# Kernel tuning notes

Hardware: AMD Instinct MI355X
Metric: run time of the kernel (lower is better)

Reference implementation:

```python
import jax, jax.numpy as jnp
import numpy as np

B, S, F, H, P = 2048, 168, 7, 128, 96  # batch, window, features, hidden, pred_len


def setup_inputs() -> dict:
    key = jax.random.key(0)
    ks = jax.random.split(key, 16)
    sc = 0.05
    return {
        "xb": jax.random.normal(ks[0], (B, S, F), dtype=jnp.float32),
        # encoder LSTM (1 layer, unidirectional); gate order i,f,g,o like torch
        "W_ih_enc": jax.random.normal(ks[1], (4 * H, F), dtype=jnp.float32) * sc,
        "W_hh_enc": jax.random.normal(ks[2], (4 * H, H), dtype=jnp.float32) * sc,
        "b_ih_enc": jax.random.normal(ks[3], (4 * H,), dtype=jnp.float32) * sc,
        "b_hh_enc": jax.random.normal(ks[4], (4 * H,), dtype=jnp.float32) * sc,
        # attention linear: (H+F) -> S
        "W_att": jax.random.normal(ks[5], (S, H + F), dtype=jnp.float32) * sc,
        "b_att": jax.random.normal(ks[6], (S,), dtype=jnp.float32) * sc,
        # decoder LSTMCell: input_size=H, hidden=H
        "W_ih_dec": jax.random.normal(ks[7], (4 * H, H), dtype=jnp.float32) * sc,
        "W_hh_dec": jax.random.normal(ks[8], (4 * H, H), dtype=jnp.float32) * sc,
        "b_ih_dec": jax.random.normal(ks[9], (4 * H,), dtype=jnp.float32) * sc,
        "b_hh_dec": jax.random.normal(ks[10], (4 * H,), dtype=jnp.float32) * sc,
        # out linear: H -> F
        "W_out": jax.random.normal(ks[11], (F, H), dtype=jnp.float32) * sc,
        "b_out": jax.random.normal(ks[12], (F,), dtype=jnp.float32) * sc,
        # final linear (output_size==1 branch): F -> 1
        "W_fin": jax.random.normal(ks[13], (1, F), dtype=jnp.float32) * sc,
        "b_fin": jax.random.normal(ks[14], (1,), dtype=jnp.float32) * sc,
    }


def _gates(pre):
    i, f, g, o = jnp.split(pre, 4, axis=-1)
    return jax.nn.sigmoid(i), jax.nn.sigmoid(f), jnp.tanh(g), jax.nn.sigmoid(o)


def _forward(xb, W_ih_enc, W_hh_enc, b_ih_enc, b_hh_enc, W_att, b_att,
             W_ih_dec, W_hh_dec, b_ih_dec, b_hh_dec, W_out, b_out, W_fin, b_fin):
    b_enc = b_ih_enc + b_hh_enc
    x_ih = jnp.einsum('bsf,gf->sbg', xb, W_ih_enc)  # precompute input projections [S,B,4H]

    def enc_step(carry, xg):
        h, c = carry
        i, f, g, o = _gates(xg + h @ W_hh_enc.T + b_enc)
        c = f * c + i * g
        h = o * jnp.tanh(c)
        return (h, c), h

    h0 = jnp.zeros((xb.shape[0], W_hh_enc.shape[1]), dtype=xb.dtype)
    (h_T, _), enc_hs = jax.lax.scan(enc_step, (h0, h0), x_ih)
    encoder_output = jnp.transpose(enc_hs, (1, 0, 2))  # [B,S,H]

    b_dec = b_ih_dec + b_hh_dec

    def dec_step(carry, _):
        prev_h, y_prev = carry
        attn_in = jnp.concatenate([prev_h, y_prev], axis=1)          # [B,H+F]
        attn_w = jax.nn.softmax(attn_in @ W_att.T + b_att, axis=-1)  # [B,S]
        combine = jnp.einsum('bs,bsh->bh', attn_w, encoder_output)   # [B,H]
        # torch code: rnn_hidden, rnn_hidden = cell(combine, (prev_h, prev_h))
        # -> the CELL state c' is what survives; h'/output gate discarded.
        i, f, g, _ = _gates(combine @ W_ih_dec.T + prev_h @ W_hh_dec.T + b_dec)
        c_new = f * prev_h + i * g
        out = c_new @ W_out.T + b_out                                # [B,F]
        return (c_new, out), out

    y0 = xb[:, -1, :]
    _, outs = jax.lax.scan(dec_step, (h_T, y0), None, length=P)      # [P,B,F]
    outputs = jnp.transpose(outs, (1, 0, 2))                         # [B,P,F]
    return outputs @ W_fin.T + b_fin                                 # [B,P,1]


def reference(xb, W_ih_enc, W_hh_enc, b_ih_enc, b_hh_enc, W_att, b_att,
              W_ih_dec, W_hh_dec, b_ih_dec, b_hh_dec, W_out, b_out, W_fin, b_fin):
    return _forward(xb, W_ih_enc, W_hh_enc, b_ih_enc, b_hh_enc, W_att, b_att,
                    W_ih_dec, W_hh_dec, b_ih_dec, b_hh_dec, W_out, b_out, W_fin, b_fin)
```

## Files before the change

### kernel.cpp

```cpp
#include <hip/hip_runtime.h>
#include <hip/hip_fp8.h>

#define NB   2048
#define SEQ  168
#define NF   7
#define NH   128
#define NP   96
#define EROWS 8
#define DROWS 8
#define NTHR 512
#define KE   160
#define KD   256
#define HXS  168
#define CTS  264
#define LS4  30

typedef _Float16 h16;
typedef _Float16 h16x8 __attribute__((ext_vector_type(8)));
typedef float    f32x2 __attribute__((ext_vector_type(2)));
typedef float    f32x4 __attribute__((ext_vector_type(4)));
typedef unsigned int u32x4 __attribute__((ext_vector_type(4)));

__device__ __forceinline__ void mfma_av(f32x4& acc, h16x8 a, const h16x8& b_agpr) {
  asm("v_mfma_f32_16x16x32_f16 %0, %1, %2, %0"
      : "+v"(acc) : "v"(a), "a"(b_agpr));
}
#define PIN_A(x) asm volatile("" : "+a"(x))

__device__ __forceinline__ float sigm(float x) { return 1.f / (1.f + __expf(-x)); }
__device__ __forceinline__ float tanh_(float x) {
  float e = __expf(-2.f * fabsf(x));
  return copysignf((1.f - e) / (1.f + e), x);
}

template <bool HI>
__device__ __forceinline__ unsigned int pack2_fp8(float a, float b, unsigned int old) {
#if __has_builtin(__builtin_amdgcn_cvt_pk_fp8_f32)
  return (unsigned int)__builtin_amdgcn_cvt_pk_fp8_f32(a, b, (int)old, HI);
#else
  __hip_fp8_e4m3 qa(a), qb(b);
  unsigned int pair = (unsigned int)(*(unsigned char*)&qa) |
                      ((unsigned int)(*(unsigned char*)&qb) << 8);
  return HI ? ((old & 0x0000ffffu) | (pair << 16)) : ((old & 0xffff0000u) | pair);
#endif
}
template <bool HI>
__device__ __forceinline__ f32x2 unp2(unsigned int w) {
#if __has_builtin(__builtin_amdgcn_cvt_pk_f32_fp8)
  return __builtin_amdgcn_cvt_pk_f32_fp8(w, HI);
#else
  __hip_fp8_e4m3 a, b;
  constexpr unsigned int sh = HI ? 16 : 0;
  *(unsigned char*)&a = (w >> sh) & 0xff;
  *(unsigned char*)&b = (w >> (sh + 8)) & 0xff;
  f32x2 r; r.x = (float)a; r.y = (float)b; return r;
#endif
}

constexpr size_t WENC_OFF   = 0;
constexpr size_t WDEC_OFF   = 163840;
constexpr size_t WEFF_OFF   = 425984;
constexpr size_t BEFF_OFF   = 468992;
constexpr size_t WCOMB_OFF  = 469760;
constexpr size_t BCONST_OFF = 470272;
constexpr size_t BENC_OFF   = 470528;
constexpr size_t BDEC_OFF   = 472576;
constexpr size_t ENC2_OFF   = 31981568;
constexpr size_t HT_OFF     = 44564480;

constexpr int HIST_OFF   = 0;
constexpr int CATH_OFF   = 122880;
constexpr int ATTW_OFF   = 131328;
constexpr int WAT2_OFF   = 136704;
constexpr int D0_OFF     = 146944;
constexpr int OUTP_OFF   = 152320;
constexpr int YH_OFF     = 152576;
constexpr int OBUF_OFF   = 152832;
constexpr int DSMEM      = 153088;
constexpr int SHHX_OFF = 122880;

__global__ void setup_weights(const float* __restrict__ Wih_enc, const float* __restrict__ Whh_enc,
                              const float* __restrict__ Wih_dec, const float* __restrict__ Whh_dec,
                              const float* __restrict__ Watt, const float* __restrict__ batt,
                              const float* __restrict__ Wout, const float* __restrict__ bout,
                              const float* __restrict__ Wfin, const float* __restrict__ bfin,
                              const float* __restrict__ bihe, const float* __restrict__ bhhe,
                              const float* __restrict__ bihd, const float* __restrict__ bhhd,
                              char* __restrict__ ws) {
  int idx = blockIdx.x * blockDim.x + threadIdx.x;
  constexpr int A0 = 81920;
  constexpr int A1 = A0 + 131072;
  constexpr int A2 = A1 + 21504;
  constexpr int A3 = A2 + 168;
  constexpr int A4 = A3 + 128;
  constexpr int A5 = A4 + 1;
  constexpr int A6 = A5 + 512;
  if (idx < A0) {
    int n = idx / KE, k = idx % KE;
    float v = 0.f;
    if (k < NF) v = Wih_enc[n * NF + k];
    else if (k >= 8 && k < 136) v = Whh_enc[n * NH + (k - 8)];
    ((h16*)(ws + WENC_OFF))[idx] = (h16)v;
  } else if (idx < A1) {
    int i = idx - A0;
    int n = i / KD, k = i % KD;
    float v = (k < NH) ? Wih_dec[n * NH + k] : Whh_dec[n * NH + (k - NH)];
    ((h16*)(ws + WDEC_OFF))[i] = (h16)v;
  } else if (idx < A2) {
    int i = idx - A1;
    int s = i / NH, k = i % NH;
    float v = Watt[s * (NH + NF) + k];
    #pragma unroll
    for (int f = 0; f < NF; ++f)
      v += Watt[s * (NH + NF) + NH + f] * Wout[f * NH + k];
    ((h16*)(ws + WEFF_OFF))[i] = (h16)v;
  } else if (idx < A3) {
    int s = idx - A2;
    float v = batt[s];
    #pragma unroll
    for (int f = 0; f < NF; ++f)
      v += Watt[s * (NH + NF) + NH + f] * bout[f];
    ((float*)(ws + BEFF_OFF))[s] = v;
  } else if (idx < A4) {
    int k = idx - A3;
    float v = 0.f;
    #pragma unroll
    for (int f = 0; f < NF; ++f) v += Wfin[f] * Wout[f * NH + k];
    ((float*)(ws + WCOMB_OFF))[k] = v;
  } else if (idx < A5) {
    float v = bfin[0];
    #pragma unroll
    for (int f = 0; f < NF; ++f) v += bout[f] * Wfin[f];
    ((float*)(ws + BCONST_OFF))[0] = v;
  } else if (idx < A6) {
    int g = idx - A5;
    ((float*)(ws + BENC_OFF))[g] = bihe[g] + bhhe[g];
    ((float*)(ws + BDEC_OFF))[g] = bihd[g] + bhhd[g];
  }
}

__global__ __attribute__((amdgpu_flat_work_group_size(NTHR, NTHR), amdgpu_waves_per_eu(2, 2)))
void fused_kernel(const float* __restrict__ xb, const h16* __restrict__ w16enc,
                  const float* __restrict__ bencp, unsigned int* __restrict__ encw2,
                  float* __restrict__ hTg,
                  const float* __restrict__ Watt, const float* __restrict__ Wout,
                  const float* __restrict__ bout,
                  const h16* __restrict__ w16dec, const h16* __restrict__ weff,
                  const float* __restrict__ beffp, const float* __restrict__ wcombp,
                  const float* __restrict__ bconstp, const float* __restrict__ bdecp,
                  float* __restrict__ out) {
  extern __shared__ char smem[];
  unsigned int* hist = (unsigned int*)(smem + HIST_OFF);
  h16 (*sh_hx)[16][HXS] = (h16(*)[16][HXS])(smem + SHHX_OFF);
  h16*   sh_cath  = (h16*)(smem + CATH_OFF);
  float* sh_attw  = (float*)(smem + ATTW_OFF);
  h16*   sh_watt2 = (h16*)(smem + WAT2_OFF);
  float* sh_d0    = (float*)(smem + D0_OFF);
  float* sh_outp  = (float*)(smem + OUTP_OFF);
  float* sh_yh    = (float*)(smem + YH_OFF);
  float* sh_obuf  = (float*)(smem + OBUF_OFF);

  const int t  = threadIdx.x;
  const int r0 = blockIdx.x * EROWS;

  const int w  = t >> 6;
  const int l  = t & 63;
  const int lq = l >> 4;
  const int ln = l & 15;
  const int hcol = w * 16 + ln;
  const int mrow = lq * 4;
  const bool act = (lq < 2);

  const int j  = t & 3;
  const int rf = t >> 2;
  const int xr = rf / NF;
  const int xf = rf - xr * NF;

  for (int i = t; i < 2 * 16 * HXS; i += NTHR) ((h16*)sh_hx)[i] = (h16)0.f;

  h16x8 bfE[4][5];
  float bE[4];
  #pragma unroll
  for (int g = 0; g < 4; ++g) {
    int n = g * 128 + hcol;
    bE[g] = bencp[n];
    #pragma unroll
    for (int kt = 0; kt < 5; ++kt) {
      bfE[g][kt] = *(const h16x8*)(w16enc + n * KE + kt * 32 + lq * 8);
      PIN_A(bfE[g][kt]);
    }
  }
  __syncthreads();
  if (t < EROWS * NF) {
    int r = t / NF, f = t - (t / NF) * NF;
    sh_hx[0][r][f] = (h16)xb[((size_t)(r0 + r) * SEQ + 0) * NF + f];
  }

  float creg[4] = {0.f, 0.f, 0.f, 0.f};
  float hstate[4] = {0.f, 0.f, 0.f, 0.f};
  float hprev[4] = {0.f, 0.f, 0.f, 0.f};
  unsigned int hpack[4] = {0u, 0u, 0u, 0u};
  float xstash = 0.f;

  __syncthreads();

  for (int s = 0; s < SEQ; ++s) {
    const int cur = s & 1;
    if ((s & 3) == 0 && t < EROWS * NF * 4) {
      int sx = s + 1 + j;
      xstash = (sx < SEQ) ? xb[((size_t)(r0 + xr) * SEQ + sx) * NF + xf] : 0.f;
    }

    f32x4 ac[4] = {{0.f,0.f,0.f,0.f},{0.f,0.f,0.f,0.f},{0.f,0.f,0.f,0.f},{0.f,0.f,0.f,0.f}};
    #pragma unroll
    for (int kt = 0; kt < 5; ++kt) {
      h16x8 af = *(const h16x8*)(&sh_hx[cur][ln][kt * 32 + lq * 8]);
      #pragma unroll
      for (int g = 0; g < 4; ++g)
        mfma_av(ac[g], af, bfE[g][kt]);
    }

    if (act) {
      #pragma unroll
      for (int reg = 0; reg < 4; ++reg) {
        float gi = sigm(ac[0][reg] + bE[0]);
        float gf = sigm(ac[1][reg] + bE[1]);
        float gg = tanh_(ac[2][reg] + bE[2]);
        float go = sigm(ac[3][reg] + bE[3]);
        float c = gf * creg[reg] + gi * gg;
        creg[reg] = c;
        float h = go * tanh_(c);
        hstate[reg] = h;
        sh_hx[cur ^ 1][mrow + reg][8 + hcol] = (h16)h;
        float hs = h * 16.f;
        if ((s & 1) == 0) hprev[reg] = hs;
        else if ((s & 3) == 1) hpack[reg] = pack2_fp8<false>(hprev[reg], hs, hpack[reg]);
        else                   hpack[reg] = pack2_fp8<true>(hprev[reg], hs, hpack[reg]);
      }
      if ((s & 3) == 3) {
        int s4 = s >> 2;
        if (s4 < LS4) {
          #pragma unroll
          for (int reg = 0; reg < 4; ++reg)
            hist[(size_t)(mrow + reg) * (LS4 * NH) + s4 * NH + hcol] = hpack[reg];
        } else {
          int q = s4 - LS4;
          #pragma unroll
          for (int reg = 0; reg < 4; ++reg)
            encw2[(((size_t)(r0 + mrow + reg) * 3 + (q >> 2)) * NH + hcol) * 4 + (q & 3)] = hpack[reg];
        }
      }
    }
    if (t < EROWS * NF * 4 && (s & 3) == j && s + 1 < SEQ)
      sh_hx[cur ^ 1][xr][xf] = (h16)xstash;
    __syncthreads();
  }

  if (act) {
    #pragma unroll
    for (int reg = 0; reg < 4; ++reg)
      hTg[(size_t)(r0 + mrow + reg) * NH + hcol] = hstate[reg];
  }
  __syncthreads();

  for (int i = t; i < 40 * NH; i += NTHR) sh_watt2[i] = weff[128 * NH + i];

  h16x8 bfD[3][8];
  float bD[3];
  #pragma unroll
  for (int g = 0; g < 3; ++g) {
    int n = g * 128 + hcol;
    bD[g] = bdecp[n];
    #pragma unroll
    for (int kt = 0; kt < 8; ++kt) {
      bfD[g][kt] = *(const h16x8*)(w16dec + n * KD + kt * 32 + lq * 8);
      PIN_A(bfD[g][kt]);
    }
  }
  h16x8 bfA[4];
  #pragma unroll
  for (int kt = 0; kt < 4; ++kt) {
    bfA[kt] = *(const h16x8*)(weff + hcol * NH + kt * 32 + lq * 8);
    PIN_A(bfA[kt]);
  }
  const float beffR = beffp[hcol];
  const int s2v = 128 + hcol;
  const float beff2 = (w < 3 && s2v < SEQ) ? beffp[s2v] : 0.f;
  const float wcombR = wcombp[hcol];
  const float bconstv = bconstp[0];

  if (act) {
    #pragma unroll
    for (int reg = 0; reg < 4; ++reg) {
      creg[reg] = hstate[reg];
      sh_cath[0 * 8 * CTS + (mrow + reg) * CTS + 128 + hcol] = (h16)hstate[reg];
    }
  }
  if (t < DROWS * NF) {
    int r = t / NF, f = t - (t / NF) * NF;
    float a = bout[f];
    const float* wr = Wout + f * NH;
    const float* hp = hTg + (size_t)(r0 + r) * NH;
    #pragma unroll 8
    for (int k = 0; k < NH; k += 4) {
      float4 pv = *(const float4*)(hp + k);
      float4 wv = *(const float4*)(wr + k);
      a += pv.x * wv.x + pv.y * wv.y + pv.z * wv.z + pv.w * wv.w;
    }
    sh_yh[t] = a;
  }
  __syncthreads();
  for (int i = t; i < DROWS * SEQ; i += NTHR) {
    int r = i / SEQ, s = i - (i / SEQ) * SEQ;
    float a = 0.f;
    #pragma unroll
    for (int f = 0; f < NF; ++f) {
      float y0f = xb[((size_t)(r0 + r) * SEQ + (SEQ - 1)) * NF + f];
      a += (y0f - sh_yh[r * NF + f]) * Watt[s * (NH + NF) + NH + f];
    }
    sh_d0[i] = a;
  }

  const int dr = t >> 7;
  const int dh = t & 127;
  const unsigned int* hrowA = hist + (size_t)dr * (LS4 * NH) + dh;
  const unsigned int* hrowB = hist + (size_t)(dr + 4) * (LS4 * NH) + dh;
  const float* erowA = sh_attw + dr * SEQ;
  const float* erowB = sh_attw + (dr + 4) * SEQ;

  u32x4 tA[3], tB[3];
  {
    const u32x4* e2 = (const u32x4*)encw2;
    #pragma unroll
    for (int b = 0; b < 3; ++b) {
      tA[b] = e2[((size_t)(r0 + dr)     * 3 + b) * NH + dh];
      tB[b] = e2[((size_t)(r0 + dr + 4) * 3 + b) * NH + dh];
    }
  }
  __syncthreads();

  for (int p = 0; p < NP; ++p) {
    const int CA = p & 1;

    if (p > 0 && t < DROWS) {
      float a = bconstv;
      #pragma unroll
      for (int w2 = 0; w2 < 8; ++w2) a += sh_outp[w2 * 8 + t];
      int slot = (p - 1) & 7;
      sh_obuf[t * 8 + slot] = a;
      if (slot == 7) {
        int base = p - 8;
        #pragma unroll
        for (int jj = 0; jj < 8; ++jj)
          out[(size_t)(r0 + t) * NP + base + jj] = sh_obuf[t * 8 + jj];
      }
    }

    {
      h16x8 afA[4];
      #pragma unroll
      for (int kt = 0; kt < 4; ++kt)
        afA[kt] = *(const h16x8*)(sh_cath + CA * 8 * CTS + (ln & 7) * CTS + 128 + kt * 32 + lq * 8);
      f32x4 acc = {0.f, 0.f, 0.f, 0.f};
      #pragma unroll
      for (int kt = 0; kt < 4; ++kt)
        mfma_av(acc, afA[kt], bfA[kt]);
      if (act) {
        #pragma unroll
        for (int reg = 0; reg < 4; ++reg) {
          int row = mrow + reg;
          float lg = acc[reg] + beffR;
          if (p == 0) lg += sh_d0[row * SEQ + hcol];
          lg = fminf(fmaxf(lg, -30.f), 30.f);
          sh_attw[row * SEQ + hcol] = __expf(lg);
        }
      }
      if (w < 3) {
        int srow = (s2v < SEQ ? s2v : SEQ - 1) - 128;
        f32x4 acc2 = {0.f, 0.f, 0.f, 0.f};
        #pragma unroll
        for (int kt = 0; kt < 4; ++kt) {
          h16x8 bf2 = *(const h16x8*)(sh_watt2 + srow * NH + kt * 32 + lq * 8);
          acc2 = __builtin_amdgcn_mfma_f32_16x16x32_f16(afA[kt], bf2, acc2, 0, 0, 0);
        }
        if (s2v < SEQ && act) {
          #pragma unroll
          for (int reg = 0; reg < 4; ++reg) {
            int row = mrow + reg;
            float lg = acc2[reg] + beff2;
            if (p == 0) lg += sh_d0[row * SEQ + s2v];
            lg = fminf(fmaxf(lg, -30.f), 30.f);
            sh_attw[row * SEQ + s2v] = __expf(lg);
          }
        }
      }
    }
    __syncthreads();

    {
      float dA = erowA[l] + erowA[64 + l];
      float dB = erowB[l] + erowB[64 + l];
      if (l < SEQ - 128) { dA += erowA[128 + l]; dB += erowB[128 + l]; }
      #pragma unroll
      for (int k = 1; k < 64; k <<= 1) {
        dA += __shfl_xor(dA, k);
        dB += __shfl_xor(dB, k);
      }
      const float invA = 0.0625f / dA;
      const float invB = 0.0625f / dB;

      f32x2 avA = {0.f, 0.f};
      f32x2 avB = {0.f, 0.f};
      #pragma unroll 6
      for (int s4 = 0; s4 < LS4; ++s4) {
        unsigned int evA = hrowA[s4 * NH];
        unsigned int evB = hrowB[s4 * NH];
        float4 eA = *(const float4*)(erowA + s4 * 4);
        float4 eB = *(const float4*)(erowB + s4 * 4);
        f32x2 wA01 = {eA.x, eA.y}, wA23 = {eA.z, eA.w};
        f32x2 wB01 = {eB.x, eB.y}, wB23 = {eB.z, eB.w};
        avA = wA01 * unp2<false>(evA) + avA;
        avA = wA23 * unp2<true>(evA) + avA;
        avB = wB01 * unp2<false>(evB) + avB;
        avB = wB23 * unp2<true>(evB) + avB;
      }
      #pragma unroll
      for (int b = 0; b < 3; ++b) {
        #pragma unroll
        for (int jj = 0; jj < 4; ++jj) {
          int s4 = LS4 + b * 4 + jj;
          unsigned int evA = tA[b][jj];
          unsigned int evB = tB[b][jj];
          float4 eA = *(const float4*)(erowA + s4 * 4);
          float4 eB = *(const float4*)(erowB + s4 * 4);
          f32x2 wA01 = {eA.x, eA.y}, wA23 = {eA.z, eA.w};
          f32x2 wB01 = {eB.x, eB.y}, wB23 = {eB.z, eB.w};
          avA = wA01 * unp2<false>(evA) + avA;
          avA = wA23 * unp2<true>(evA) + avA;
          avB = wB01 * unp2<false>(evB) + avB;
          avB = wB23 * unp2<true>(evB) + avB;
        }
      }
      sh_cath[CA * 8 * CTS + dr * CTS + dh]       = (h16)((avA.x + avA.y) * invA);
      sh_cath[CA * 8 * CTS + (dr + 4) * CTS + dh] = (h16)((avB.x + avB.y) * invB);
    }
    __syncthreads();

    {
      f32x4 ag[3] = {{0.f,0.f,0.f,0.f},{0.f,0.f,0.f,0.f},{0.f,0.f,0.f,0.f}};
      #pragma unroll
      for (int kt = 0; kt < 8; ++kt) {
        h16x8 af = *(const h16x8*)(sh_cath + CA * 8 * CTS + (ln & 7) * CTS + kt * 32 + lq * 8);
        #pragma unroll
        for (int g = 0; g < 3; ++g)
          mfma_av(ag[g], af, bfD[g][kt]);
      }
      if (act) {
        float contrib[4];
        #pragma unroll
        for (int reg = 0; reg < 4; ++reg) {
          int row = mrow + reg;
          float gi = sigm(ag[0][reg] + bD[0]);
          float gf = sigm(ag[1][reg] + bD[1]);
          float gg = tanh_(ag[2][reg] + bD[2]);
          float cn = gf * creg[reg] + gi * gg;
          creg[reg] = cn;
          sh_cath[(CA ^ 1) * 8 * CTS + row * CTS + 128 + hcol] = (h16)cn;
          contrib[reg] = cn * wcombR;
        }
        #pragma unroll
        for (int reg = 0; reg < 4; ++reg) {
          float rsum = contrib[reg];
          rsum += __shfl_xor(rsum, 1);
          rsum += __shfl_xor(rsum, 2);
          rsum += __shfl_xor(rsum, 4);
          rsum += __shfl_xor(rsum, 8);
          if (ln == 0) sh_outp[w * 8 + mrow + reg] = rsum;
        }
      }
    }
    __syncthreads();
  }

  if (t < DROWS) {
    float a = bconstv;
    #pragma unroll
    for (int w2 = 0; w2 < 8; ++w2) a += sh_outp[w2 * 8 + t];
    sh_obuf[t * 8 + 7] = a;
    #pragma unroll
    for (int jj = 0; jj < 8; ++jj)
      out[(size_t)(r0 + t) * NP + (NP - 8) + jj] = sh_obuf[t * 8 + jj];
  }
}

extern "C" void kernel_launch(void* const* d_in, const int* in_sizes, int n_in,
                              void* d_out, int out_size, void* d_ws, size_t ws_size,
                              hipStream_t stream) {
  const float* xb      = (const float*)d_in[0];
  const float* Wih_enc = (const float*)d_in[1];
  const float* Whh_enc = (const float*)d_in[2];
  const float* bih_enc = (const float*)d_in[3];
  const float* bhh_enc = (const float*)d_in[4];
  const float* Watt    = (const float*)d_in[5];
  const float* batt    = (const float*)d_in[6];
  const float* Wih_dec = (const float*)d_in[7];
  const float* Whh_dec = (const float*)d_in[8];
  const float* bih_dec = (const float*)d_in[9];
  const float* bhh_dec = (const float*)d_in[10];
  const float* Wout    = (const float*)d_in[11];
  const float* bout    = (const float*)d_in[12];
  const float* Wfin    = (const float*)d_in[13];
  const float* bfin    = (const float*)d_in[14];
  char* ws = (char*)d_ws;

  hipFuncSetAttribute(reinterpret_cast<const void*>(fused_kernel),
                      hipFuncAttributeMaxDynamicSharedMemorySize, DSMEM);

  setup_weights<<<920, 256, 0, stream>>>(Wih_enc, Whh_enc, Wih_dec, Whh_dec,
                                         Watt, batt, Wout, bout, Wfin, bfin,
                                         bih_enc, bhh_enc, bih_dec, bhh_dec, ws);
  fused_kernel<<<NB / EROWS, NTHR, DSMEM, stream>>>(
      xb, (const h16*)(ws + WENC_OFF), (const float*)(ws + BENC_OFF),
      (unsigned int*)(ws + ENC2_OFF), (float*)(ws + HT_OFF),
      Watt, Wout, bout,
      (const h16*)(ws + WDEC_OFF), (const h16*)(ws + WEFF_OFF),
      (const float*)(ws + BEFF_OFF), (const float*)(ws + WCOMB_OFF),
      (const float*)(ws + BCONST_OFF), (const float*)(ws + BDEC_OFF),
      (float*)d_out);
}
```

Before: 905.5 us.

## Split decoder rows into two groups and software-pipeline attention and cell stages

```diff
diff --git a/kernel.cpp b/kernel.cpp
--- a/kernel.cpp
+++ b/kernel.cpp
@@ -21,9 +21,8 @@
 typedef float    f32x4 __attribute__((ext_vector_type(4)));
 typedef unsigned int u32x4 __attribute__((ext_vector_type(4)));
 
-__device__ __forceinline__ void mfma_av(f32x4& acc, h16x8 a, const h16x8& b_agpr) {
-  asm("v_mfma_f32_16x16x32_f16 %0, %1, %2, %0"
-      : "+v"(acc) : "v"(a), "a"(b_agpr));
+__device__ __forceinline__ void mfma_b(f32x4& acc, h16x8 a, h16x8 b) {
+  acc = __builtin_amdgcn_mfma_f32_16x16x32_f16(a, b, acc, 0, 0, 0);
 }
 #define PIN_A(x) asm volatile("" : "+a"(x))
 
@@ -74,9 +73,9 @@
 constexpr int WAT2_OFF   = 136704;
 constexpr int D0_OFF     = 146944;
 constexpr int OUTP_OFF   = 152320;
-constexpr int YH_OFF     = 152576;
-constexpr int OBUF_OFF   = 152832;
-constexpr int DSMEM      = 153088;
+constexpr int YH_OFF     = 152832;
+constexpr int OBUF_OFF   = 153088;
+constexpr int DSMEM      = 153344;
 constexpr int SHHX_OFF = 122880;
 
 __global__ void setup_weights(const float* __restrict__ Wih_enc, const float* __restrict__ Whh_enc,
@@ -217,7 +216,7 @@
       h16x8 af = *(const h16x8*)(&sh_hx[cur][ln][kt * 32 + lq * 8]);
       #pragma unroll
       for (int g = 0; g < 4; ++g)
-        mfma_av(ac[g], af, bfE[g][kt]);
+        mfma_b(ac[g], af, bfE[g][kt]);
     }
 
     if (act) {
@@ -289,12 +288,16 @@
   const float wcombR = wcombp[hcol];
   const float bconstv = bconstp[0];
 
+  float cregA[4], cregB[4];
+  #pragma unroll
+  for (int reg = 0; reg < 4; ++reg) {
+    cregA[reg] = hstate[reg];
+    cregB[reg] = __shfl(hstate[reg], 16 + ln);
+  }
   if (act) {
     #pragma unroll
-    for (int reg = 0; reg < 4; ++reg) {
-      creg[reg] = hstate[reg];
+    for (int reg = 0; reg < 4; ++reg)
       sh_cath[0 * 8 * CTS + (mrow + reg) * CTS + 128 + hcol] = (h16)hstate[reg];
-    }
   }
   if (t < DROWS * NF) {
     int r = t / NF, f = t - (t / NF) * NF;
@@ -339,13 +342,124 @@
   }
   __syncthreads();
 
+  auto D1g = [&](int G, int CA, bool p0) {
+    const int arow = G * 4 + (ln & 3);
+    h16x8 afA[4];
+    #pragma unroll
+    for (int kt = 0; kt < 4; ++kt)
+      afA[kt] = *(const h16x8*)(sh_cath + CA * 8 * CTS + arow * CTS + 128 + kt * 32 + lq * 8);
+    f32x4 acc = {0.f, 0.f, 0.f, 0.f};
+    #pragma unroll
+    for (int kt = 0; kt < 4; ++kt)
+      mfma_b(acc, afA[kt], bfA[kt]);
+    if (lq == 0) {
+      #pragma unroll
+      for (int reg = 0; reg < 4; ++reg) {
+        int row = G * 4 + reg;
+        float lg = acc[reg] + beffR;
+        if (p0) lg += sh_d0[row * SEQ + hcol];
+        lg = fminf(fmaxf(lg, -30.f), 30.f);
+        sh_attw[row * SEQ + hcol] = __expf(lg);
+      }
+    }
+    if (w < 3) {
+      int srow = (s2v < SEQ ? s2v : SEQ - 1) - 128;
+      f32x4 acc2 = {0.f, 0.f, 0.f, 0.f};
+      #pragma unroll
+      for (int kt = 0; kt < 4; ++kt) {
+        h16x8 bf2 = *(const h16x8*)(sh_watt2 + srow * NH + kt * 32 + lq * 8);
+        mfma_b(acc2, afA[kt], bf2);
+      }
+      if (s2v < SEQ && lq == 0) {
+        #pragma unroll
+        for (int reg = 0; reg < 4; ++reg) {
+          int row = G * 4 + reg;
+          float lg = acc2[reg] + beff2;
+          if (p0) lg += sh_d0[row * SEQ + s2v];
+          lg = fminf(fmaxf(lg, -30.f), 30.f);
+          sh_attw[row * SEQ + s2v] = __expf(lg);
+        }
+      }
+    }
+  };
+
+  auto D3g = [&](int G, int CA, const u32x4* treg, const unsigned int* hrow, const float* erow) {
+    float d = erow[l] + erow[64 + l];
+    if (l < SEQ - 128) d += erow[128 + l];
+    #pragma unroll
+    for (int k = 1; k < 64; k <<= 1) d += __shfl_xor(d, k);
+    const float inv = 0.0625f / d;
+
+    f32x2 av = {0.f, 0.f};
+    #pragma unroll 6
+    for (int s4 = 0; s4 < LS4; ++s4) {
+      unsigned int ev = hrow[s4 * NH];
+      float4 e4 = *(const float4*)(erow + s4 * 4);
+      f32x2 w01 = {e4.x, e4.y}, w23 = {e4.z, e4.w};
+      av = w01 * unp2<false>(ev) + av;
+      av = w23 * unp2<true>(ev) + av;
+    }
+    #pragma unroll
+    for (int b = 0; b < 3; ++b) {
+      #pragma unroll
+      for (int jj = 0; jj < 4; ++jj) {
+        int s4 = LS4 + b * 4 + jj;
+        unsigned int ev = treg[b][jj];
+        float4 e4 = *(const float4*)(erow + s4 * 4);
+        f32x2 w01 = {e4.x, e4.y}, w23 = {e4.z, e4.w};
+        av = w01 * unp2<false>(ev) + av;
+        av = w23 * unp2<true>(ev) + av;
+      }
+    }
+    sh_cath[CA * 8 * CTS + (G * 4 + dr) * CTS + dh] = (h16)((av.x + av.y) * inv);
+  };
+
+  auto D4g = [&](int G, int CA, float* cregG, int p) {
+    const int arow = G * 4 + (ln & 3);
+    f32x4 ag[3] = {{0.f,0.f,0.f,0.f},{0.f,0.f,0.f,0.f},{0.f,0.f,0.f,0.f}};
+    #pragma unroll
+    for (int kt = 0; kt < 8; ++kt) {
+      h16x8 af = *(const h16x8*)(sh_cath + CA * 8 * CTS + arow * CTS + kt * 32 + lq * 8);
+      #pragma unroll
+      for (int g = 0; g < 3; ++g)
+        mfma_b(ag[g], af, bfD[g][kt]);
+    }
+    if (lq == 0) {
+      float contrib[4];
+      #pragma unroll
+      for (int reg = 0; reg < 4; ++reg) {
+        int row = G * 4 + reg;
+        float gi = sigm(ag[0][reg] + bD[0]);
+        float gf = sigm(ag[1][reg] + bD[1]);
+        float gg = tanh_(ag[2][reg] + bD[2]);
+        float cn = gf * cregG[reg] + gi * gg;
+        cregG[reg] = cn;
+        sh_cath[(CA ^ 1) * 8 * CTS + row * CTS + 128 + hcol] = (h16)cn;
+        contrib[reg] = cn * wcombR;
+      }
+      #pragma unroll
+      for (int reg = 0; reg < 4; ++reg) {
+        float rsum = contrib[reg];
+        rsum += __shfl_xor(rsum, 1);
+        rsum += __shfl_xor(rsum, 2);
+        rsum += __shfl_xor(rsum, 4);
+        rsum += __shfl_xor(rsum, 8);
+        if (ln == 0) sh_outp[(p & 1) * 64 + w * 8 + G * 4 + reg] = rsum;
+      }
+    }
+  };
+
   for (int p = 0; p < NP; ++p) {
     const int CA = p & 1;
 
+    if (p > 0) D4g(1, (p - 1) & 1, cregB, p - 1);
+    D1g(0, CA, p == 0);
+    __syncthreads();
+
     if (p > 0 && t < DROWS) {
       float a = bconstv;
       #pragma unroll
-      for (int w2 = 0; w2 < 8; ++w2) a += sh_outp[w2 * 8 + t];
+      for (int w2 = 0; w2 < 8; ++w2) a += sh_outp[((p - 1) & 1) * 64 + w2 * 8 + t];
       int slot = (p - 1) & 7;
       sh_obuf[t * 8 + slot] = a;
       if (slot == 7) {
@@ -355,137 +469,21 @@
           out[(size_t)(r0 + t) * NP + base + jj] = sh_obuf[t * 8 + jj];
       }
     }
-
-    {
-      h16x8 afA[4];
-      #pragma unroll
-      for (int kt = 0; kt < 4; ++kt)
-        afA[kt] = *(const h16x8*)(sh_cath + CA * 8 * CTS + (ln & 7) * CTS + 128 + kt * 32 + lq * 8);
-      f32x4 acc = {0.f, 0.f, 0.f, 0.f};
-      #pragma unroll
-      for (int kt = 0; kt < 4; ++kt)
-        mfma_av(acc, afA[kt], bfA[kt]);
-      if (act) {
-        #pragma unroll
-        for (int reg = 0; reg < 4; ++reg) {
-          int row = mrow + reg;
-          float lg = acc[reg] + beffR;
-          if (p == 0) lg += sh_d0[row * SEQ + hcol];
-          lg = fminf(fmaxf(lg, -30.f), 30.f);
-          sh_attw[row * SEQ + hcol] = __expf(lg);
-        }
-      }
-      if (w < 3) {
-        int srow = (s2v < SEQ ? s2v : SEQ - 1) - 128;
-        f32x4 acc2 = {0.f, 0.f, 0.f, 0.f};
-        #pragma unroll
-        for (int kt = 0; kt < 4; ++kt) {
-          h16x8 bf2 = *(const h16x8*)(sh_watt2 + srow * NH + kt * 32 + lq * 8);
-          acc2 = __builtin_amdgcn_mfma_f32_16x16x32_f16(afA[kt], bf2, acc2, 0, 0, 0);
-        }
-        if (s2v < SEQ && act) {
-          #pragma unroll
-          for (int reg = 0; reg < 4; ++reg) {
-            int row = mrow + reg;
-            float lg = acc2[reg] + beff2;
-            if (p == 0) lg += sh_d0[row * SEQ + s2v];
-            lg = fminf(fmaxf(lg, -30.f), 30.f);
-            sh_attw[row * SEQ + s2v] = __expf(lg);
-          }
-        }
-      }
-    }
+    D1g(1, CA, p == 0);
+    D3g(0, CA, tA, hrowA, erowA);
     __syncthreads();
 
-    {
-      float dA = erowA[l] + erowA[64 + l];
-      float dB = erowB[l] + erowB[64 + l];
-      if (l < SEQ - 128) { dA += erowA[128 + l]; dB += erowB[128 + l]; }
-      #pragma unroll
-      for (int k = 1; k < 64; k <<= 1) {
-        dA += __shfl_xor(dA, k);
-        dB += __shfl_xor(dB, k);
-      }
-      const float invA = 0.0625f / dA;
-      const float invB = 0.0625f / dB;
-
-      f32x2 avA = {0.f, 0.f};
-      f32x2 avB = {0.f, 0.f};
-      #pragma unroll 6
-      for (int s4 = 0; s4 < LS4; ++s4) {
-        unsigned int evA = hrowA[s4 * NH];
-        unsigned int evB = hrowB[s4 * NH];
-        float4 eA = *(const float4*)(erowA + s4 * 4);
-        float4 eB = *(const float4*)(erowB + s4 * 4);
-        f32x2 wA01 = {eA.x, eA.y}, wA23 = {eA.z, eA.w};
-        f32x2 wB01 = {eB.x, eB.y}, wB23 = {eB.z, eB.w};
-        avA = wA01 * unp2<false>(evA) + avA;
-        avA = wA23 * unp2<true>(evA) + avA;
-        avB = wB01 * unp2<false>(evB) + avB;
-        avB = wB23 * unp2<true>(evB) + avB;
-      }
-      #pragma unroll
-      for (int b = 0; b < 3; ++b) {
-        #pragma unroll
-        for (int jj = 0; jj < 4; ++jj) {
-          int s4 = LS4 + b * 4 + jj;
-          unsigned int evA = tA[b][jj];
-          unsigned int evB = tB[b][jj];
-          float4 eA = *(const float4*)(erowA + s4 * 4);
-          float4 eB = *(const float4*)(erowB + s4 * 4);
-          f32x2 wA01 = {eA.x, eA.y}, wA23 = {eA.z, eA.w};
-          f32x2 wB01 = {eB.x, eB.y}, wB23 = {eB.z, eB.w};
-          avA = wA01 * unp2<false>(evA) + avA;
-          avA = wA23 * unp2<true>(evA) + avA;
-          avB = wB01 * unp2<false>(evB) + avB;
-          avB = wB23 * unp2<true>(evB) + avB;
-        }
-      }
-      sh_cath[CA * 8 * CTS + dr * CTS + dh]       = (h16)((avA.x + avA.y) * invA);
-      sh_cath[CA * 8 * CTS + (dr + 4) * CTS + dh] = (h16)((avB.x + avB.y) * invB);
-    }
+    D3g(1, CA, tB, hrowB, erowB);
+    D4g(0, CA, cregA, p);
     __syncthreads();
-
-    {
-      f32x4 ag[3] = {{0.f,0.f,0.f,0.f},{0.f,0.f,0.f,0.f},{0.f,0.f,0.f,0.f}};
-      #pragma unroll
-      for (int kt = 0; kt < 8; ++kt) {
-        h16x8 af = *(const h16x8*)(sh_cath + CA * 8 * CTS + (ln & 7) * CTS + kt * 32 + lq * 8);
-        #pragma unroll
-        for (int g = 0; g < 3; ++g)
-          mfma_av(ag[g], af, bfD[g][kt]);
-      }
-      if (act) {
-        float contrib[4];
-        #pragma unroll
-        for (int reg = 0; reg < 4; ++reg) {
-          int row = mrow + reg;
-          float gi = sigm(ag[0][reg] + bD[0]);
-          float gf = sigm(ag[1][reg] + bD[1]);
-          float gg = tanh_(ag[2][reg] + bD[2]);
-          float cn = gf * creg[reg] + gi * gg;
-          creg[reg] = cn;
-          sh_cath[(CA ^ 1) * 8 * CTS + row * CTS + 128 + hcol] = (h16)cn;
-          contrib[reg] = cn * wcombR;
-        }
-        #pragma unroll
-        for (int reg = 0; reg < 4; ++reg) {
-          float rsum = contrib[reg];
-          rsum += __shfl_xor(rsum, 1);
-          rsum += __shfl_xor(rsum, 2);
-          rsum += __shfl_xor(rsum, 4);
-          rsum += __shfl_xor(rsum, 8);
-          if (ln == 0) sh_outp[w * 8 + mrow + reg] = rsum;
-        }
-      }
-    }
-    __syncthreads();
-  }
-
+  }
+
+  D4g(1, (NP - 1) & 1, cregB, NP - 1);
+  __syncthreads();
   if (t < DROWS) {
     float a = bconstv;
     #pragma unroll
-    for (int w2 = 0; w2 < 8; ++w2) a += sh_outp[w2 * 8 + t];
+    for (int w2 = 0; w2 < 8; ++w2) a += sh_outp[((NP - 1) & 1) * 64 + w2 * 8 + t];
     sh_obuf[t * 8 + 7] = a;
     #pragma unroll
     for (int jj = 0; jj < 8; ++jj)
```

Measured after the change: 1.376 ms. 1.52x slower.
